# Kernel tuning notes

Measured on AMD Instinct MI355X. Metric: run time of the kernel, lower is better.

The kernel has to match this reference:

```python
import jax, jax.numpy as jnp
import numpy as np

D_MODEL = 2048
N_EXPERTS = 64
TOP_K = 8
N_TOKENS = 16384


def setup_inputs() -> dict:
    key = jax.random.key(0)
    k1, k2 = jax.random.split(key)
    x_flat = jax.random.normal(k1, (N_TOKENS, D_MODEL), dtype=jnp.float32)
    # nn.Linear(d_model, n_experts) weight has shape [n_experts, d_model]
    gate_w = jax.random.normal(k2, (N_EXPERTS, D_MODEL), dtype=jnp.float32) * (1.0 / np.sqrt(D_MODEL))
    return {"x_flat": x_flat, "gate_w": gate_w}


def reference(x_flat, gate_w):
    # logits = x_flat @ gate_w.T : [tokens, n_experts]
    logits = jnp.einsum("td,ed->te", x_flat, gate_w)
    full_probs = jax.nn.softmax(logits, axis=-1)
    topk_logits, topk_idx = jax.lax.top_k(logits, TOP_K)
    topk_weights = jax.nn.softmax(topk_logits, axis=-1)
    return topk_idx, topk_weights, full_probs, logits
```

## Files before the change

kernel.cpp:

```cpp
#include <hip/hip_runtime.h>
#include <math.h>

#define D_MODEL   2048
#define N_EXPERTS 64
#define TOP_K     8
#define N_TOKENS  16384
#define TOK_TILE  16
#define NTHREADS  256
#define NCHUNK    32
#define WS_NEED   (64*4*3*64*16)

typedef __attribute__((ext_vector_type(8))) short bf16x8;
typedef __attribute__((ext_vector_type(4))) float f32x4;
typedef __attribute__((ext_vector_type(4))) int   i32x4;

union FragU { i32x4 i; bf16x8 h; };

__device__ __forceinline__ void split3(float x, unsigned &h, unsigned &m, unsigned &l) {
    unsigned ux = __float_as_uint(x);
    h = ux & 0xffff0000u;
    float mf = x - __uint_as_float(h);
    unsigned um = __float_as_uint(mf) & 0xffff0000u;
    float lf = mf - __uint_as_float(um);
    m = um;
    l = __float_as_uint(lf) & 0xffff0000u;
}

__device__ __forceinline__ void async_cp16(const float* g, float* l) {
    __builtin_amdgcn_global_load_lds(
        (const __attribute__((address_space(1))) void*)g,
        (__attribute__((address_space(3))) void*)l, 16, 0, 0);
}

__global__ __launch_bounds__(256) void pack_w_kernel(const float* __restrict__ gw,
                                                     unsigned* __restrict__ wp) {
    const int g    = blockIdx.x * 256 + threadIdx.x;
    const int d    = g & 3;
    const int lane = (g >> 2) & 63;
    const int rest = g >> 8;
    const int v    = rest % 3;
    const int t    = rest / 3;
    const int fr   = t & 3;
    const int ks   = t >> 2;
    const int e    = fr * 16 + (lane & 15);
    const int k    = ks * 32 + (lane >> 4) * 8 + 2 * d;
    const float w0 = gw[(size_t)e * D_MODEL + k];
    const float w1 = gw[(size_t)e * D_MODEL + k + 1];
    unsigned h0, m0, l0, h1, m1, l1;
    split3(w0, h0, m0, l0);
    split3(w1, h1, m1, l1);
    const unsigned c0 = (v == 0) ? h0 : ((v == 1) ? m0 : l0);
    const unsigned c1 = (v == 0) ? h1 : ((v == 1) ? m1 : l1);
    wp[g] = (c0 >> 16) | c1;
}

__device__ __forceinline__ void splitpack(const float4 a, const float4 b,
                                          FragU &ph, FragU &pm, FragU &pl) {
    const float f[8] = {a.x, a.y, a.z, a.w, b.x, b.y, b.z, b.w};
#pragma unroll
    for (int d = 0; d < 4; ++d) {
        unsigned h0, m0, l0, h1, m1, l1;
        split3(f[2 * d],     h0, m0, l0);
        split3(f[2 * d + 1], h1, m1, l1);
        ph.i[d] = (int)((h0 >> 16) | h1);
        pm.i[d] = (int)((m0 >> 16) | m1);
        pl.i[d] = (int)((l0 >> 16) | l1);
    }
}

#define MFMA(A_, B_, C_) C_ = __builtin_amdgcn_mfma_f32_16x16x32_bf16((A_).h, (B_).h, C_, 0, 0, 0)

#define CHUNK_BODY(c, bufi, DO_STAGE, sbuf)                                  \
    {                                                                        \
        const unsigned* bt0_ = wb + (size_t)(2 * (c)) * 3072;                \
        const unsigned* bt1_ = bt0_ + 3072;                                  \
        const i32x4 B0h = *(const i32x4*)(bt0_ +   0);                       \
        const i32x4 B0m = *(const i32x4*)(bt0_ + 256);                       \
        const i32x4 B0l = *(const i32x4*)(bt0_ + 512);                       \
        const i32x4 B1h = *(const i32x4*)(bt1_ +   0);                       \
        const i32x4 B1m = *(const i32x4*)(bt1_ + 256);                       \
        const i32x4 B1l = *(const i32x4*)(bt1_ + 512);                       \
        const float* xb_ = xsflat + (bufi) * LBUF;                           \
        const float4 Aa0 = *(const float4*)(xb_ + offa0);                    \
        const float4 Ab0 = *(const float4*)(xb_ + offb0);                    \
        FragU ah, am_, al;                                                   \
        splitpack(Aa0, Ab0, ah, am_, al);                                    \
        FragU bh, bm, bl;                                                    \
        bh.i = B0h; bm.i = B0m; bl.i = B0l;                                  \
        MFMA(ah, bh, accA); MFMA(am_, bh, accA); MFMA(al, bh, accA);         \
        MFMA(ah, bm, accB); MFMA(am_, bm, accB); MFMA(ah, bl, accB);         \
        if (DO_STAGE)                                                        \
            async_cp16(srcx + ((c) + 2) * 64, ldst + (sbuf) * LBUF);         \
        const float4 Aa1 = *(const float4*)(xb_ + offa1);                    \
        const float4 Ab1 = *(const float4*)(xb_ + offb1);                    \
        splitpack(Aa1, Ab1, ah, am_, al);                                    \
        bh.i = B1h; bm.i = B1m; bl.i = B1l;                                  \
        MFMA(ah, bh, accA); MFMA(am_, bh, accA); MFMA(al, bh, accA);         \
        MFMA(ah, bm, accB); MFMA(am_, bm, accB); MFMA(ah, bl, accB);         \
        __builtin_amdgcn_s_barrier();                                        \
    }

__global__ __launch_bounds__(NTHREADS, 4) void router_mfma(
    const float* __restrict__ x, const unsigned* __restrict__ wp,
    float* __restrict__ out)
{
    __shared__ __align__(16) float xs[3][TOK_TILE][64];
    __shared__ float lt[TOK_TILE][N_EXPERTS + 1];
    __shared__ float smax[TOK_TILE], srs[TOK_TILE];

    const int tid  = threadIdx.x;
    const int lane = tid & 63;
    const int wv   = tid >> 6;
    const int m0   = blockIdx.x * TOK_TILE;

    const int lrow = lane & 15;
    const int lk   = lane >> 4;

    float* xsflat = &xs[0][0][0];
    const int LBUF = TOK_TILE * 64;

    const int rowx = wv * 4 + lk;
    const float* srcx = x + (size_t)(m0 + rowx) * D_MODEL
                        + 4 * ((lane & 15) ^ (rowx & 7));
    float* ldst = xsflat + wv * 256;

    const int am0  = lrow & 7;
    const int offa0 = lrow * 64 + 4 * (( 2 * lk)     ^ am0);
    const int offb0 = lrow * 64 + 4 * (( 2 * lk + 1) ^ am0);
    const int offa1 = lrow * 64 + 4 * ((8 + 2 * lk)     ^ am0);
    const int offb1 = lrow * 64 + 4 * ((8 + 2 * lk + 1) ^ am0);

    const unsigned* wb = wp + (size_t)(wv * 3) * 256 + lane * 4;

    f32x4 accA = {0.f, 0.f, 0.f, 0.f};
    f32x4 accB = accA;

    async_cp16(srcx,      ldst + 0 * LBUF);
    async_cp16(srcx + 64, ldst + 1 * LBUF);
    asm volatile("s_waitcnt vmcnt(1)" ::: "memory");
    __builtin_amdgcn_s_barrier();

    for (int cc = 0; cc < 30; cc += 3) {
        CHUNK_BODY(cc + 0, 0, 1, 2);
        CHUNK_BODY(cc + 1, 1, 1, 0);
        CHUNK_BODY(cc + 2, 2, 1, 1);
    }
    CHUNK_BODY(30, 0, 0, 0);
    CHUNK_BODY(31, 1, 0, 0);

#undef CHUNK_BODY

#pragma unroll
    for (int r = 0; r < 4; ++r)
        lt[lk * 4 + r][wv * 16 + lrow] = accA[r] + accB[r];
    __syncthreads();

    float* out_idx = out;
    float* out_w   = out + (size_t)N_TOKENS * TOP_K;
    float* out_p   = out + (size_t)2 * N_TOKENS * TOP_K;
    float* out_l   = out_p + (size_t)N_TOKENS * N_EXPERTS;

    if (tid < TOK_TILE) {
        const int t = tid;
        float tv[TOP_K];
        int   ti[TOP_K];
#pragma unroll
        for (int i = 0; i < TOP_K; ++i) { tv[i] = -INFINITY; ti[i] = 0; }
        float m = -INFINITY;

        for (int e = 0; e < N_EXPERTS; ++e) {
            const float v = lt[t][e];
            m = fmaxf(m, v);
            if (v > tv[TOP_K - 1]) {
#pragma unroll
                for (int j = TOP_K - 1; j >= 1; --j) {
                    const bool shift = (v > tv[j - 1]);
                    const bool here  = (v > tv[j]);
                    const float ntv = shift ? tv[j - 1] : (here ? v : tv[j]);
                    const int   nti = shift ? ti[j - 1] : (here ? e : ti[j]);
                    tv[j] = ntv; ti[j] = nti;
                }
                if (v > tv[0]) { tv[0] = v; ti[0] = e; }
            }
        }

        float s = 0.f;
        for (int e = 0; e < N_EXPERTS; ++e) s += expf(lt[t][e] - m);
        const float rs = 1.f / s;
        smax[t] = m;
        srs[t]  = rs;

        float ex[TOP_K];
        float wsum = 0.f;
#pragma unroll
        for (int i = 0; i < TOP_K; ++i) { ex[i] = expf(tv[i] - tv[0]); wsum += ex[i]; }
        const float rw = 1.f / wsum;

        const int tok = m0 + t;
#pragma unroll
        for (int i = 0; i < TOP_K; ++i) {
            out_idx[(size_t)tok * TOP_K + i] = (float)ti[i];
            out_w  [(size_t)tok * TOP_K + i] = ex[i] * rw;
        }
    }
    __syncthreads();

    {
        const int f = tid * 4;
        const int t = f >> 6;
        const int e = f & 63;
        const float l0 = lt[t][e + 0];
        const float l1 = lt[t][e + 1];
        const float l2 = lt[t][e + 2];
        const float l3 = lt[t][e + 3];
        const float mm = smax[t];
        const float rr = srs[t];
        float4 pv = make_float4(expf(l0 - mm) * rr, expf(l1 - mm) * rr,
                                expf(l2 - mm) * rr, expf(l3 - mm) * rr);
        float4 lv = make_float4(l0, l1, l2, l3);
        const size_t gbase = (size_t)m0 * N_EXPERTS + f;
        *(float4*)(out_p + gbase) = pv;
        *(float4*)(out_l + gbase) = lv;
    }
}

__global__ __launch_bounds__(512) void router_fallback(
    const float* __restrict__ x, const float* __restrict__ gw,
    float* __restrict__ out)
{
    __shared__ float xs[64][33];
    __shared__ float wsh[N_EXPERTS][36];
    __shared__ float lt[64][N_EXPERTS + 1];
    __shared__ float smax[64], srs[64];

    const int tid  = threadIdx.x;
    const int lane = tid & 63;
    const int wv   = tid >> 6;
    const int m0   = blockIdx.x * 64;
    const int srow = tid >> 3;
    const int skq  = (tid & 7) * 4;

    const float* xsrc = x  + (size_t)(m0 + srow) * D_MODEL + skq;
    const float* wsrc = gw + (size_t)srow        * D_MODEL + skq;
    float4 xr = *(const float4*)(xsrc);
    float4 wr = *(const float4*)(wsrc);

    float acc[8];
#pragma unroll
    for (int i = 0; i < 8; ++i) acc[i] = 0.f;
    const int e0 = wv * 8;

    for (int c = 0; c < D_MODEL / 32; ++c) {
        xs[srow][skq] = xr.x; xs[srow][skq+1] = xr.y; xs[srow][skq+2] = xr.z; xs[srow][skq+3] = xr.w;
        *(float4*)&wsh[srow][skq] = wr;
        __syncthreads();
        if (c + 1 < D_MODEL / 32) {
            xr = *(const float4*)(xsrc + (c + 1) * 32);
            wr = *(const float4*)(wsrc + (c + 1) * 32);
        }
#pragma unroll 8
        for (int k4 = 0; k4 < 8; ++k4) {
            const float4 xv = *(const float4*)&xs[lane][k4 * 4];
#pragma unroll
            for (int e = 0; e < 8; ++e) {
                const float4 w4 = *(const float4*)&wsh[e0 + e][k4 * 4];
                acc[e] = fmaf(xv.x, w4.x, fmaf(xv.y, w4.y, fmaf(xv.z, w4.z, fmaf(xv.w, w4.w, acc[e]))));
            }
        }
        __syncthreads();
    }
#pragma unroll
    for (int e = 0; e < 8; ++e) lt[lane][e0 + e] = acc[e];
    __syncthreads();

    float* out_idx = out;
    float* out_w   = out + (size_t)N_TOKENS * TOP_K;
    float* out_p   = out + (size_t)2 * N_TOKENS * TOP_K;
    float* out_l   = out_p + (size_t)N_TOKENS * N_EXPERTS;

    if (tid < 64) {
        const int t = tid;
        float tv[TOP_K]; int ti[TOP_K];
#pragma unroll
        for (int i = 0; i < TOP_K; ++i) { tv[i] = -INFINITY; ti[i] = 0; }
        float m = -INFINITY;
        for (int e = 0; e < N_EXPERTS; ++e) {
            const float v = lt[t][e];
            m = fmaxf(m, v);
            if (v > tv[TOP_K - 1]) {
#pragma unroll
                for (int j = TOP_K - 1; j >= 1; --j) {
                    const bool shift = (v > tv[j - 1]);
                    const bool here  = (v > tv[j]);
                    const float ntv = shift ? tv[j - 1] : (here ? v : tv[j]);
                    const int   nti = shift ? ti[j - 1] : (here ? e : ti[j]);
                    tv[j] = ntv; ti[j] = nti;
                }
                if (v > tv[0]) { tv[0] = v; ti[0] = e; }
            }
        }
        float s = 0.f;
        for (int e = 0; e < N_EXPERTS; ++e) s += expf(lt[t][e] - m);
        const float rs = 1.f / s;
        smax[t] = m; srs[t] = rs;
        float ex[TOP_K]; float wsum = 0.f;
#pragma unroll
        for (int i = 0; i < TOP_K; ++i) { ex[i] = expf(tv[i] - tv[0]); wsum += ex[i]; }
        const float rw = 1.f / wsum;
        const int tok = m0 + t;
#pragma unroll
        for (int i = 0; i < TOP_K; ++i) {
            out_idx[(size_t)tok * TOP_K + i] = (float)ti[i];
            out_w  [(size_t)tok * TOP_K + i] = ex[i] * rw;
        }
    }
    __syncthreads();
#pragma unroll
    for (int rep = 0; rep < 2; ++rep) {
        const int f = rep * (512 * 4) + tid * 4;
        const int t = f >> 6;
        const int e = f & 63;
        const float l0 = lt[t][e], l1 = lt[t][e+1], l2 = lt[t][e+2], l3 = lt[t][e+3];
        const float mm = smax[t], rr = srs[t];
        float4 pv = make_float4(expf(l0-mm)*rr, expf(l1-mm)*rr, expf(l2-mm)*rr, expf(l3-mm)*rr);
        float4 lv = make_float4(l0, l1, l2, l3);
        const size_t gbase = (size_t)m0 * N_EXPERTS + f;
        *(float4*)(out_p + gbase) = pv;
        *(float4*)(out_l + gbase) = lv;
    }
}

extern "C" void kernel_launch(void* const* d_in, const int* in_sizes, int n_in,
                              void* d_out, int out_size, void* d_ws, size_t ws_size,
                              hipStream_t stream) {
    const float* x  = (const float*)d_in[0];
    const float* gw = (const float*)d_in[1];
    float* out = (float*)d_out;
    if (ws_size >= (size_t)WS_NEED) {
        unsigned* wp = (unsigned*)d_ws;
        pack_w_kernel<<<dim3(WS_NEED / 4 / 256), dim3(256), 0, stream>>>(gw, wp);
        router_mfma<<<dim3(N_TOKENS / TOK_TILE), dim3(NTHREADS), 0, stream>>>(x, wp, out);
    } else {
        router_fallback<<<dim3(N_TOKENS / 64), dim3(512), 0, stream>>>(x, gw, out);
    }
}
```

Before: 83.24 us.

## Enlarge token tile to 64 and stage pre-split A and B fragments in LDS

Raises the token tile from 16 to 64 with 1024 threads (16 waves arranged 4 row groups by 4 expert groups). Each x element is now split into bf16 hi/mid/lo once and written to LDS, and the packed weight fragments are also staged into LDS via async copies with triple buffering. This removes the redundant per-wave x splitting and the per-block global weight reads, so weight traffic is amortized over more tokens. In exchange it uses about 144KB of LDS and large blocks, which limits occupancy and gives fewer blocks (256) across the CUs. The register prefetch of x also adds extra staging work each chunk.

```diff
diff --git a/kernel.cpp b/kernel.cpp
--- a/kernel.cpp
+++ b/kernel.cpp
@@ -5,10 +5,14 @@
 #define N_EXPERTS 64
 #define TOP_K     8
 #define N_TOKENS  16384
-#define TOK_TILE  16
-#define NTHREADS  256
+#define TOK_TILE  64
+#define NTHREADS  1024
 #define NCHUNK    32
-#define WS_NEED   (64*4*3*64*16)
+#define WS_NEED   (32*24576)
+
+#define A_BUF     24576
+#define B_REGION  73728
+#define SMEM_BYTES 147456
 
 typedef __attribute__((ext_vector_type(8))) short bf16x8;
 typedef __attribute__((ext_vector_type(4))) float f32x4;
@@ -26,7 +30,7 @@
     l = __float_as_uint(lf) & 0xffff0000u;
 }
 
-__device__ __forceinline__ void async_cp16(const float* g, float* l) {
+__device__ __forceinline__ void async_cp16(const void* g, void* l) {
     __builtin_amdgcn_global_load_lds(
         (const __attribute__((address_space(1))) void*)g,
         (__attribute__((address_space(3))) void*)l, 16, 0, 0);
@@ -35,124 +39,145 @@
 __global__ __launch_bounds__(256) void pack_w_kernel(const float* __restrict__ gw,
                                                      unsigned* __restrict__ wp) {
     const int g    = blockIdx.x * 256 + threadIdx.x;
-    const int d    = g & 3;
+    const int dw   = g & 3;
     const int lane = (g >> 2) & 63;
-    const int rest = g >> 8;
-    const int v    = rest % 3;
-    const int t    = rest / 3;
-    const int fr   = t & 3;
-    const int ks   = t >> 2;
-    const int e    = fr * 16 + (lane & 15);
-    const int k    = ks * 32 + (lane >> 4) * 8 + 2 * d;
+    const int u    = g >> 8;
+    const int p    = u % 3;
+    const int v2   = u / 3;
+    const int cg   = v2 & 3;
+    const int ks   = (v2 >> 2) & 1;
+    const int chunk= v2 >> 3;
+    const int e    = cg * 16 + (lane & 15);
+    const int k    = chunk * 64 + ks * 32 + (lane >> 4) * 8 + dw * 2;
     const float w0 = gw[(size_t)e * D_MODEL + k];
     const float w1 = gw[(size_t)e * D_MODEL + k + 1];
     unsigned h0, m0, l0, h1, m1, l1;
     split3(w0, h0, m0, l0);
     split3(w1, h1, m1, l1);
-    const unsigned c0 = (v == 0) ? h0 : ((v == 1) ? m0 : l0);
-    const unsigned c1 = (v == 0) ? h1 : ((v == 1) ? m1 : l1);
+    const unsigned c0 = (p == 0) ? h0 : ((p == 1) ? m0 : l0);
+    const unsigned c1 = (p == 0) ? h1 : ((p == 1) ? m1 : l1);
     wp[g] = (c0 >> 16) | c1;
 }
 
-__device__ __forceinline__ void splitpack(const float4 a, const float4 b,
-                                          FragU &ph, FragU &pm, FragU &pl) {
-    const float f[8] = {a.x, a.y, a.z, a.w, b.x, b.y, b.z, b.w};
-#pragma unroll
-    for (int d = 0; d < 4; ++d) {
-        unsigned h0, m0, l0, h1, m1, l1;
-        split3(f[2 * d],     h0, m0, l0);
-        split3(f[2 * d + 1], h1, m1, l1);
-        ph.i[d] = (int)((h0 >> 16) | h1);
-        pm.i[d] = (int)((m0 >> 16) | m1);
-        pl.i[d] = (int)((l0 >> 16) | l1);
-    }
+__device__ __forceinline__ void conv_write(const float4 v, char* p0) {
+    unsigned h0,m0_,l0, h1,m1,l1, h2,m2,l2, h3,m3,l3;
+    split3(v.x, h0, m0_, l0);
+    split3(v.y, h1, m1, l1);
+    split3(v.z, h2, m2, l2);
+    split3(v.w, h3, m3, l3);
+    uint2 hw, mw, lw;
+    hw.x = (h0 >> 16) | h1;  hw.y = (h2 >> 16) | h3;
+    mw.x = (m0_>> 16) | m1;  mw.y = (m2 >> 16) | m3;
+    lw.x = (l0 >> 16) | l1;  lw.y = (l2 >> 16) | l3;
+    *(uint2*)(p0)        = hw;
+    *(uint2*)(p0 + 1024) = mw;
+    *(uint2*)(p0 + 2048) = lw;
 }
 
 #define MFMA(A_, B_, C_) C_ = __builtin_amdgcn_mfma_f32_16x16x32_bf16((A_).h, (B_).h, C_, 0, 0, 0)
-
-#define CHUNK_BODY(c, bufi, DO_STAGE, sbuf)                                  \
-    {                                                                        \
-        const unsigned* bt0_ = wb + (size_t)(2 * (c)) * 3072;                \
-        const unsigned* bt1_ = bt0_ + 3072;                                  \
-        const i32x4 B0h = *(const i32x4*)(bt0_ +   0);                       \
-        const i32x4 B0m = *(const i32x4*)(bt0_ + 256);                       \
-        const i32x4 B0l = *(const i32x4*)(bt0_ + 512);                       \
-        const i32x4 B1h = *(const i32x4*)(bt1_ +   0);                       \
-        const i32x4 B1m = *(const i32x4*)(bt1_ + 256);                       \
-        const i32x4 B1l = *(const i32x4*)(bt1_ + 512);                       \
-        const float* xb_ = xsflat + (bufi) * LBUF;                           \
-        const float4 Aa0 = *(const float4*)(xb_ + offa0);                    \
-        const float4 Ab0 = *(const float4*)(xb_ + offb0);                    \
-        FragU ah, am_, al;                                                   \
-        splitpack(Aa0, Ab0, ah, am_, al);                                    \
-        FragU bh, bm, bl;                                                    \
-        bh.i = B0h; bm.i = B0m; bl.i = B0l;                                  \
-        MFMA(ah, bh, accA); MFMA(am_, bh, accA); MFMA(al, bh, accA);         \
-        MFMA(ah, bm, accB); MFMA(am_, bm, accB); MFMA(ah, bl, accB);         \
-        if (DO_STAGE)                                                        \
-            async_cp16(srcx + ((c) + 2) * 64, ldst + (sbuf) * LBUF);         \
-        const float4 Aa1 = *(const float4*)(xb_ + offa1);                    \
-        const float4 Ab1 = *(const float4*)(xb_ + offb1);                    \
-        splitpack(Aa1, Ab1, ah, am_, al);                                    \
-        bh.i = B1h; bm.i = B1m; bl.i = B1l;                                  \
-        MFMA(ah, bh, accA); MFMA(am_, bh, accA); MFMA(al, bh, accA);         \
-        MFMA(ah, bm, accB); MFMA(am_, bm, accB); MFMA(ah, bl, accB);         \
-        __builtin_amdgcn_s_barrier();                                        \
-    }
 
 __global__ __launch_bounds__(NTHREADS, 4) void router_mfma(
     const float* __restrict__ x, const unsigned* __restrict__ wp,
     float* __restrict__ out)
 {
-    __shared__ __align__(16) float xs[3][TOK_TILE][64];
-    __shared__ float lt[TOK_TILE][N_EXPERTS + 1];
-    __shared__ float smax[TOK_TILE], srs[TOK_TILE];
+    __shared__ __align__(16) char smem[SMEM_BYTES];
 
     const int tid  = threadIdx.x;
     const int lane = tid & 63;
-    const int wv   = tid >> 6;
+    const int w    = tid >> 6;
     const int m0   = blockIdx.x * TOK_TILE;
 
+    const int r    = w & 3;
+    const int cg   = w >> 2;
     const int lrow = lane & 15;
     const int lk   = lane >> 4;
 
-    float* xsflat = &xs[0][0][0];
-    const int LBUF = TOK_TILE * 64;
-
-    const int rowx = wv * 4 + lk;
-    const float* srcx = x + (size_t)(m0 + rowx) * D_MODEL
-                        + 4 * ((lane & 15) ^ (rowx & 7));
-    float* ldst = xsflat + wv * 256;
-
-    const int am0  = lrow & 7;
-    const int offa0 = lrow * 64 + 4 * (( 2 * lk)     ^ am0);
-    const int offb0 = lrow * 64 + 4 * (( 2 * lk + 1) ^ am0);
-    const int offa1 = lrow * 64 + 4 * ((8 + 2 * lk)     ^ am0);
-    const int offb1 = lrow * 64 + 4 * ((8 + 2 * lk + 1) ^ am0);
-
-    const unsigned* wb = wp + (size_t)(wv * 3) * 256 + lane * 4;
+    const int sk  = (tid >> 9) & 1;
+    const int srg = (tid >> 7) & 3;
+    const int sln = (tid >> 1) & 63;
+    const int sh  = tid & 1;
+    const float* xsrc = x + (size_t)(m0 + srg * 16 + (sln & 15)) * D_MODEL
+                        + sk * 32 + (sln >> 4) * 8 + sh * 4;
+    const int aw0 = (sk * 4 + srg) * 3072 + sln * 16 + sh * 8;
+
+    const int j0 = (2 * w) % 24, j1 = (2 * w + 1) % 24;
+    const char* wsrc0 = (const char*)wp + j0 * 1024 + lane * 16;
+    const char* wsrc1 = (const char*)wp + j1 * 1024 + lane * 16;
+
+    const int aofs = r  * 3072 + lane * 16;
+    const int bofs = B_REGION + cg * 3072 + lane * 16;
 
     f32x4 accA = {0.f, 0.f, 0.f, 0.f};
     f32x4 accB = accA;
 
-    async_cp16(srcx,      ldst + 0 * LBUF);
-    async_cp16(srcx + 64, ldst + 1 * LBUF);
-    asm volatile("s_waitcnt vmcnt(1)" ::: "memory");
-    __builtin_amdgcn_s_barrier();
-
-    for (int cc = 0; cc < 30; cc += 3) {
-        CHUNK_BODY(cc + 0, 0, 1, 2);
-        CHUNK_BODY(cc + 1, 1, 1, 0);
-        CHUNK_BODY(cc + 2, 2, 1, 1);
-    }
-    CHUNK_BODY(30, 0, 0, 0);
-    CHUNK_BODY(31, 1, 0, 0);
-
-#undef CHUNK_BODY
-
-#pragma unroll
-    for (int r = 0; r < 4; ++r)
-        lt[lk * 4 + r][wv * 16 + lrow] = accA[r] + accB[r];
+#define STAGE_AND_WAIT(c, CUR, NXT, WAITSTR)                                   \
+    {                                                                          \
+        if ((c) + 1 < NCHUNK) {                                                \
+            const int bw_ = ((c) + 1) % 3;                                     \
+            char* bb_ = smem + B_REGION + bw_ * 24576;                         \
+             \
+            async_cp16(wsrc0 + ((c) + 1) * 24576, bb_ + j0 * 1024);            \
+            async_cp16(wsrc1 + ((c) + 1) * 24576, bb_ + j1 * 1024);            \
+            if ((c) + 2 < NCHUNK) NXT = *(const float4*)(xsrc + ((c) + 2) * 64); \
+            conv_write(CUR, smem + bw_ * A_BUF + aw0);                         \
+        }                                                                      \
+        asm volatile("s_waitcnt " WAITSTR " lgkmcnt(0)" ::: "memory");         \
+        __builtin_amdgcn_sched_barrier(0);                                     \
+        __builtin_amdgcn_s_barrier();                                          \
+        __builtin_amdgcn_sched_barrier(0);                                     \
+    }
+
+#define COMPUTE(c)                                                             \
+    {                                                                          \
+        const char* cb_ = smem + ((c) % 3) * 24576;                            \
+        _Pragma("unroll")                                                      \
+        for (int ks = 0; ks < 2; ++ks) {                                       \
+            const char* ap_ = cb_ + ks * 12288 + aofs;                         \
+            const char* bp_ = cb_ + ks * 12288 + bofs;                         \
+            FragU ah, am_, al, bh, bm, bl;                                     \
+            ah.i  = *(const i32x4*)(ap_);                                      \
+            am_.i = *(const i32x4*)(ap_ + 1024);                               \
+            al.i  = *(const i32x4*)(ap_ + 2048);                               \
+            bh.i  = *(const i32x4*)(bp_);                                      \
+            bm.i  = *(const i32x4*)(bp_ + 1024);                               \
+            bl.i  = *(const i32x4*)(bp_ + 2048);                               \
+            MFMA(ah, bh, accA); MFMA(am_, bh, accA); MFMA(al, bh, accA);       \
+            MFMA(ah, bm, accB); MFMA(am_, bm, accB); MFMA(ah, bl, accB);       \
+        }                                                                      \
+    }
+
+    float4 X, Y;
+    {
+        async_cp16(wsrc0, smem + B_REGION + j0 * 1024);
+        async_cp16(wsrc1, smem + B_REGION + j1 * 1024);
+        float4 T = *(const float4*)(xsrc);
+        X = *(const float4*)(xsrc + 64);
+        conv_write(T, smem + aw0);
+        asm volatile("s_waitcnt lgkmcnt(0)" ::: "memory");
+        __builtin_amdgcn_sched_barrier(0);
+        __builtin_amdgcn_s_barrier();
+        __builtin_amdgcn_sched_barrier(0);
+    }
+
+    for (int c = 0; c < 28; c += 2) {
+        STAGE_AND_WAIT(c,     X, Y, "vmcnt(1)"); COMPUTE(c);
+        STAGE_AND_WAIT(c + 1, Y, X, "vmcnt(1)"); COMPUTE(c + 1);
+    }
+    STAGE_AND_WAIT(28, X, Y, "vmcnt(1)"); COMPUTE(28);
+    STAGE_AND_WAIT(29, Y, X, "vmcnt(1)"); COMPUTE(29);
+    STAGE_AND_WAIT(30, X, Y, "vmcnt(2)"); COMPUTE(30);
+    STAGE_AND_WAIT(31, Y, X, "vmcnt(0)"); COMPUTE(31);
+
+#undef STAGE_AND_WAIT
+#undef COMPUTE
+
+    float (*lt)[N_EXPERTS + 1] = (float (*)[N_EXPERTS + 1])smem;
+    float* smax = (float*)smem + TOK_TILE * (N_EXPERTS + 1);
+    float* srs  = smax + TOK_TILE;
+
+#pragma unroll
+    for (int reg = 0; reg < 4; ++reg)
+        lt[r * 16 + lk * 4 + reg][cg * 16 + lrow] = accA[reg] + accB[reg];
     __syncthreads();
 
     float* out_idx = out;
```

Result: no change. 83.71 us (+0.6%).

## Split K across waves with direct register loads and LDS partial reduction

Applied to the files above, without the earlier changes.

Restructures the router GEMM so each of the four waves owns one quarter of the reduction dimension and all 64 experts, instead of one expert slice over the full K. X is loaded straight from global memory into registers with one-step software prefetch, which removes the LDS async staging, the triple buffering and the per-chunk barriers. Partial logits from the waves are summed through shared memory before the top-k/softmax epilogue. In exchange, each lane now holds eight accumulators and twelve B fragments per step, which raises register pressure, and the X loads lose the coalesced LDS staging path.

```diff
diff --git a/kernel.cpp b/kernel.cpp
--- a/kernel.cpp
+++ b/kernel.cpp
@@ -5,9 +5,7 @@
 #define N_EXPERTS 64
 #define TOP_K     8
 #define N_TOKENS  16384
-#define TOK_TILE  16
 #define NTHREADS  256
-#define NCHUNK    32
 #define WS_NEED   (64*4*3*64*16)
 
 typedef __attribute__((ext_vector_type(8))) short bf16x8;
@@ -24,12 +22,6 @@
     float lf = mf - __uint_as_float(um);
     m = um;
     l = __float_as_uint(lf) & 0xffff0000u;
-}
-
-__device__ __forceinline__ void async_cp16(const float* g, float* l) {
-    __builtin_amdgcn_global_load_lds(
-        (const __attribute__((address_space(1))) void*)g,
-        (__attribute__((address_space(3))) void*)l, 16, 0, 0);
 }
 
 __global__ __launch_bounds__(256) void pack_w_kernel(const float* __restrict__ gw,
@@ -70,97 +62,111 @@
 
 #define MFMA(A_, B_, C_) C_ = __builtin_amdgcn_mfma_f32_16x16x32_bf16((A_).h, (B_).h, C_, 0, 0, 0)
 
-#define CHUNK_BODY(c, bufi, DO_STAGE, sbuf)                                  \
+#define FRAG6(Bh_, Bm_, Bl_, ACCA_, ACCB_)                                   \
     {                                                                        \
-        const unsigned* bt0_ = wb + (size_t)(2 * (c)) * 3072;                \
-        const unsigned* bt1_ = bt0_ + 3072;                                  \
-        const i32x4 B0h = *(const i32x4*)(bt0_ +   0);                       \
-        const i32x4 B0m = *(const i32x4*)(bt0_ + 256);                       \
-        const i32x4 B0l = *(const i32x4*)(bt0_ + 512);                       \
-        const i32x4 B1h = *(const i32x4*)(bt1_ +   0);                       \
-        const i32x4 B1m = *(const i32x4*)(bt1_ + 256);                       \
-        const i32x4 B1l = *(const i32x4*)(bt1_ + 512);                       \
-        const float* xb_ = xsflat + (bufi) * LBUF;                           \
-        const float4 Aa0 = *(const float4*)(xb_ + offa0);                    \
-        const float4 Ab0 = *(const float4*)(xb_ + offb0);                    \
-        FragU ah, am_, al;                                                   \
-        splitpack(Aa0, Ab0, ah, am_, al);                                    \
-        FragU bh, bm, bl;                                                    \
-        bh.i = B0h; bm.i = B0m; bl.i = B0l;                                  \
-        MFMA(ah, bh, accA); MFMA(am_, bh, accA); MFMA(al, bh, accA);         \
-        MFMA(ah, bm, accB); MFMA(am_, bm, accB); MFMA(ah, bl, accB);         \
-        if (DO_STAGE)                                                        \
-            async_cp16(srcx + ((c) + 2) * 64, ldst + (sbuf) * LBUF);         \
-        const float4 Aa1 = *(const float4*)(xb_ + offa1);                    \
-        const float4 Ab1 = *(const float4*)(xb_ + offb1);                    \
-        splitpack(Aa1, Ab1, ah, am_, al);                                    \
-        bh.i = B1h; bm.i = B1m; bl.i = B1l;                                  \
-        MFMA(ah, bh, accA); MFMA(am_, bh, accA); MFMA(al, bh, accA);         \
-        MFMA(ah, bm, accB); MFMA(am_, bm, accB); MFMA(ah, bl, accB);         \
-        __builtin_amdgcn_s_barrier();                                        \
+        FragU bh_, bm_, bl_;                                                 \
+        bh_.i = Bh_; bm_.i = Bm_; bl_.i = Bl_;                               \
+        MFMA(ah, bh_, ACCA_); MFMA(am_, bh_, ACCA_); MFMA(al, bh_, ACCA_);   \
+        MFMA(ah, bm_, ACCB_); MFMA(am_, bm_, ACCB_); MFMA(ah, bl_, ACCB_);   \
     }
 
 __global__ __launch_bounds__(NTHREADS, 4) void router_mfma(
     const float* __restrict__ x, const unsigned* __restrict__ wp,
     float* __restrict__ out)
 {
-    __shared__ __align__(16) float xs[3][TOK_TILE][64];
-    __shared__ float lt[TOK_TILE][N_EXPERTS + 1];
-    __shared__ float smax[TOK_TILE], srs[TOK_TILE];
+    __shared__ __align__(16) float part[4 * 1088 + 32];
 
     const int tid  = threadIdx.x;
     const int lane = tid & 63;
-    const int wv   = tid >> 6;
-    const int m0   = blockIdx.x * TOK_TILE;
+    const int q    = tid >> 6;
+    const int m0   = blockIdx.x * 16;
 
     const int lrow = lane & 15;
     const int lk   = lane >> 4;
 
-    float* xsflat = &xs[0][0][0];
-    const int LBUF = TOK_TILE * 64;
-
-    const int rowx = wv * 4 + lk;
-    const float* srcx = x + (size_t)(m0 + rowx) * D_MODEL
-                        + 4 * ((lane & 15) ^ (rowx & 7));
-    float* ldst = xsflat + wv * 256;
-
-    const int am0  = lrow & 7;
-    const int offa0 = lrow * 64 + 4 * (( 2 * lk)     ^ am0);
-    const int offb0 = lrow * 64 + 4 * (( 2 * lk + 1) ^ am0);
-    const int offa1 = lrow * 64 + 4 * ((8 + 2 * lk)     ^ am0);
-    const int offb1 = lrow * 64 + 4 * ((8 + 2 * lk + 1) ^ am0);
-
-    const unsigned* wb = wp + (size_t)(wv * 3) * 256 + lane * 4;
-
-    f32x4 accA = {0.f, 0.f, 0.f, 0.f};
-    f32x4 accB = accA;
-
-    async_cp16(srcx,      ldst + 0 * LBUF);
-    async_cp16(srcx + 64, ldst + 1 * LBUF);
-    asm volatile("s_waitcnt vmcnt(1)" ::: "memory");
-    __builtin_amdgcn_s_barrier();
-
-    for (int cc = 0; cc < 30; cc += 3) {
-        CHUNK_BODY(cc + 0, 0, 1, 2);
-        CHUNK_BODY(cc + 1, 1, 1, 0);
-        CHUNK_BODY(cc + 2, 2, 1, 1);
-    }
-    CHUNK_BODY(30, 0, 0, 0);
-    CHUNK_BODY(31, 1, 0, 0);
-
-#undef CHUNK_BODY
-
-#pragma unroll
-    for (int r = 0; r < 4; ++r)
-        lt[lk * 4 + r][wv * 16 + lrow] = accA[r] + accB[r];
-    __syncthreads();
+    const float* xa = x + (size_t)(m0 + lrow) * D_MODEL + q * 512 + lk * 8;
+    const unsigned* wb = wp + (size_t)q * 49152 + lane * 4;
+
+    f32x4 acc0a = {0.f,0.f,0.f,0.f}, acc0b = acc0a;
+    f32x4 acc1a = acc0a, acc1b = acc0a;
+    f32x4 acc2a = acc0a, acc2b = acc0a;
+    f32x4 acc3a = acc0a, acc3b = acc0a;
+
+    float4 Aa = *(const float4*)(xa);
+    float4 Ab = *(const float4*)(xa + 4);
+
+#pragma unroll 2
+    for (int s = 0; s < 16; ++s) {
+        const unsigned* bt = wb + s * 3072;
+        const i32x4 B0h = *(const i32x4*)(bt +    0);
+        const i32x4 B0m = *(const i32x4*)(bt +  256);
+        const i32x4 B0l = *(const i32x4*)(bt +  512);
+        const i32x4 B1h = *(const i32x4*)(bt +  768);
+        const i32x4 B1m = *(const i32x4*)(bt + 1024);
+        const i32x4 B1l = *(const i32x4*)(bt + 1280);
+        const i32x4 B2h = *(const i32x4*)(bt + 1536);
+        const i32x4 B2m = *(const i32x4*)(bt + 1792);
+        const i32x4 B2l = *(const i32x4*)(bt + 2048);
+        const i32x4 B3h = *(const i32x4*)(bt + 2304);
+        const i32x4 B3m = *(const i32x4*)(bt + 2560);
+        const i32x4 B3l = *(const i32x4*)(bt + 2816);
+
+        float4 Na = Aa, Nb = Ab;
+        if (s + 1 < 16) {
+            Na = *(const float4*)(xa + (s + 1) * 32);
+            Nb = *(const float4*)(xa + (s + 1) * 32 + 4);
+        }
+
+        FragU ah, am_, al;
+        splitpack(Aa, Ab, ah, am_, al);
+
+        FRAG6(B0h, B0m, B0l, acc0a, acc0b);
+        FRAG6(B1h, B1m, B1l, acc1a, acc1b);
+        FRAG6(B2h, B2m, B2l, acc2a, acc2b);
+        FRAG6(B3h, B3m, B3l, acc3a, acc3b);
+
+        Aa = Na; Ab = Nb;
+    }
+
+    {
+        float* ps = part + q * 1088;
+#pragma unroll
+        for (int reg = 0; reg < 4; ++reg) {
+            const int tok = lk * 4 + reg;
+            ps[tok * 68 +  0 + lrow] = acc0a[reg] + acc0b[reg];
+            ps[tok * 68 + 16 + lrow] = acc1a[reg] + acc1b[reg];
+            ps[tok * 68 + 32 + lrow] = acc2a[reg] + acc2b[reg];
+            ps[tok * 68 + 48 + lrow] = acc3a[reg] + acc3b[reg];
+        }
+    }
+    __syncthreads();
+
+    {
+        const int tok = tid >> 4;
+        const int e0  = (tid & 15) * 4;
+        const int o   = tok * 68 + e0;
+        float4 s0 = *(const float4*)(part + 0 * 1088 + o);
+        float4 s1 = *(const float4*)(part + 1 * 1088 + o);
+        float4 s2 = *(const float4*)(part + 2 * 1088 + o);
+        float4 s3 = *(const float4*)(part + 3 * 1088 + o);
+        float4 r = make_float4(s0.x + s1.x + s2.x + s3.x,
+                               s0.y + s1.y + s2.y + s3.y,
+                               s0.z + s1.z + s2.z + s3.z,
+                               s0.w + s1.w + s2.w + s3.w);
+        *(float4*)(part + o) = r;
+    }
+    __syncthreads();
+
+    float* lt   = part;
+    float* smax = part + 4 * 1088;
+    float* srs  = smax + 16;
 
     float* out_idx = out;
     float* out_w   = out + (size_t)N_TOKENS * TOP_K;
     float* out_p   = out + (size_t)2 * N_TOKENS * TOP_K;
     float* out_l   = out_p + (size_t)N_TOKENS * N_EXPERTS;
 
-    if (tid < TOK_TILE) {
+    if (tid < 16) {
         const int t = tid;
         float tv[TOP_K];
         int   ti[TOP_K];
@@ -169,7 +175,7 @@
         float m = -INFINITY;
 
         for (int e = 0; e < N_EXPERTS; ++e) {
-            const float v = lt[t][e];
+            const float v = lt[t * 68 + e];
             m = fmaxf(m, v);
             if (v > tv[TOP_K - 1]) {
 #pragma unroll
@@ -185,7 +191,7 @@
         }
 
         float s = 0.f;
-        for (int e = 0; e < N_EXPERTS; ++e) s += expf(lt[t][e] - m);
+        for (int e = 0; e < N_EXPERTS; ++e) s += expf(lt[t * 68 + e] - m);
         const float rs = 1.f / s;
         smax[t] = m;
         srs[t]  = rs;
@@ -209,10 +215,10 @@
         const int f = tid * 4;
         const int t = f >> 6;
         const int e = f & 63;
-        const float l0 = lt[t][e + 0];
-        const float l1 = lt[t][e + 1];
-        const float l2 = lt[t][e + 2];
-        const float l3 = lt[t][e + 3];
+        const float l0 = lt[t * 68 + e + 0];
+        const float l1 = lt[t * 68 + e + 1];
+        const float l2 = lt[t * 68 + e + 2];
+        const float l3 = lt[t * 68 + e + 3];
         const float mm = smax[t];
         const float rr = srs[t];
         float4 pv = make_float4(expf(l0 - mm) * rr, expf(l1 - mm) * rr,
@@ -339,7 +345,7 @@
     if (ws_size >= (size_t)WS_NEED) {
         unsigned* wp = (unsigned*)d_ws;
         pack_w_kernel<<<dim3(WS_NEED / 4 / 256), dim3(256), 0, stream>>>(gw, wp);
-        router_mfma<<<dim3(N_TOKENS / TOK_TILE), dim3(NTHREADS), 0, stream>>>(x, wp, out);
+        router_mfma<<<dim3(N_TOKENS / 16), dim3(NTHREADS), 0, stream>>>(x, wp, out);
     } else {
         router_fallback<<<dim3(N_TOKENS / 64), dim3(512), 0, stream>>>(x, gw, out);
     }
```

After: 81.78 us. About the same (-1.8%).
